# Kernel optimization log

Measured on AMD Instinct MI355X. Metric: run time of the kernel, lower is better.

## Reference

```python
import jax, jax.numpy as jnp
import numpy as np

B, N, D = 8, 4096, 256   # batch, nodes, input = hidden = output dim
TD, GD, L = 64, 73, 2    # topo_dim, gdv_dim, num_passes
NEG = -1e9               # fp32 mask value from get_mask_value


def setup_inputs() -> dict:
    key = jax.random.key(0)
    ks = jax.random.split(key, 24)
    s = 0.05
    nrm = lambda k, shp: jax.random.normal(k, shp, jnp.float32) * s
    d = {}
    d['x'] = jax.random.normal(ks[0], (B, N, D), jnp.float32)
    d['adj'] = jax.random.randint(ks[1], (D, D), 0, 2, jnp.int32)
    d['gdv'] = jax.random.uniform(ks[2], (D, GD), dtype=jnp.float32)
    d['W_in'] = nrm(ks[3], (D, D));   d['b_in'] = nrm(ks[4], (D,))
    d['W_out'] = nrm(ks[5], (D, D)); d['b_out'] = nrm(ks[6], (D,))
    d['g1_W'] = nrm(ks[7], (GD, TD));  d['g1_b'] = nrm(ks[8], (TD,))
    d['g2_W'] = nrm(ks[9], (TD, TD));  d['g2_b'] = nrm(ks[10], (TD,))
    d['gres_W'] = nrm(ks[11], (GD, TD)); d['gres_b'] = nrm(ks[12], (TD,))
    d['ln_g'] = jnp.ones((D,), jnp.float32); d['ln_b'] = jnp.zeros((D,), jnp.float32)
    d['Wf'] = nrm(ks[13], (L, D, D)); d['bf'] = nrm(ks[14], (L, D))
    d['Wt'] = nrm(ks[15], (L, TD, D)); d['bt'] = nrm(ks[16], (L, D))
    d['wa_feat'] = nrm(ks[17], (L, 2 * D)); d['ba_feat'] = nrm(ks[18], (L,))
    d['wa_topo'] = nrm(ks[19], (L, 2 * D)); d['ba_topo'] = nrm(ks[20], (L,))
    d['Wo'] = nrm(ks[21], (L, D, D)); d['bo'] = nrm(ks[22], (L, D))
    d['lng'] = jnp.ones((L, D), jnp.float32); d['lnb'] = jnp.zeros((L, D), jnp.float32)
    return d


def _ln(x, g, b, eps=1e-5):
    m = x.mean(-1, keepdims=True)
    v = ((x - m) ** 2).mean(-1, keepdims=True)
    return (x - m) * jax.lax.rsqrt(v + eps) * g + b


def reference(x, adj, gdv, W_in, b_in, W_out, b_out, g1_W, g1_b, g2_W, g2_b,
              gres_W, gres_b, ln_g, ln_b, Wf, bf, Wt, bt, wa_feat, ba_feat,
              wa_topo, ba_topo, Wo, bo, lng, lnb):
    # GDV -> topo embedding; batch-independent, so keep it [D, TD] instead of
    # the original's broadcast [B, D, TD] (same math, no duplicated compute).
    g = gdv / (gdv.sum(1, keepdims=True) + 1e-6)
    t = jax.nn.relu(g @ g1_W + g1_b) @ g2_W + g2_b + (g @ gres_W + gres_b)  # [D, TD]
    mask = adj == 0  # [D, D]
    h = x @ W_in + b_in  # [B, N, D]
    for l in range(L):
        Tp = t @ Wt[l] + bt[l]  # [D, D] topo projection (hidden_dim == D)
        # topo_attn Linear(2D,1) on cat([T_i, T_j]) == (Tp@w_i)_i + (Tp@w_j)_j + bias
        wi, wj = wa_topo[l, :D], wa_topo[l, D:]
        e_topo = jax.nn.leaky_relu((Tp @ wi)[:, None] + (Tp @ wj)[None, :] + ba_topo[l])
        beta = jax.nn.softmax(jnp.where(mask, NEG, e_topo), axis=-1)  # [D, D]
        T_out = beta @ Tp  # [D, D]
        Hp = h @ Wf[l] + bf[l]  # [B, N, D]
        # feature_attn Linear(2D,1) on cat([H_n, T_f]) decomposed the same way
        wh, wt = wa_feat[l, :D], wa_feat[l, D:]
        e_feat = jax.nn.leaky_relu((Hp @ wh)[:, :, None] + (T_out @ wt)[None, None, :] + ba_feat[l])
        alpha = jax.nn.softmax(e_feat, axis=-1)  # [B, N, D]
        h_new = jnp.einsum('bnf,fh->bnh', alpha, T_out)
        # output proj + residual (input==output -> plain add), dropout = identity (eval)
        h = _ln(h_new @ Wo[l] + bo[l] + h, lng[l], lnb[l])
    return _ln(h @ W_out + b_out, ln_g, ln_b)
```

## Files before the change

kernel.cpp:

```cpp
#include <hip/hip_runtime.h>
#include <hip/hip_bf16.h>


typedef float f32x4 __attribute__((ext_vector_type(4)));
typedef short bf16x8 __attribute__((ext_vector_type(8)));

__device__ __forceinline__ unsigned short f2bf(float f) {
  unsigned int u = __builtin_bit_cast(unsigned int, f);
  u += 0x7FFFu + ((u >> 16) & 1u);
  return (unsigned short)(u >> 16);
}
__device__ __forceinline__ float bf2f(unsigned short u) {
  return __builtin_bit_cast(float, (unsigned int)u << 16);
}
__device__ __forceinline__ float lrelu(float x) { return x > 0.f ? x : 0.01f * x; }

template <int CTRL>
__device__ __forceinline__ float dpp_ror_add(float v) {
  int s = __builtin_amdgcn_update_dpp(0, __builtin_bit_cast(int, v), CTRL, 0xf, 0xf, true);
  return v + __builtin_bit_cast(float, s);
}
__device__ __forceinline__ float sum16(float v) {
  v = dpp_ror_add<0x128>(v);
  v = dpp_ror_add<0x124>(v);
  v = dpp_ror_add<0x122>(v);
  v = dpp_ror_add<0x121>(v);
  return v;
}

__device__ __forceinline__ float block_sum(float v, float* s4, int t) {
  v = sum16(v);
  v += __shfl_xor(v, 16, 64);
  v += __shfl_xor(v, 32, 64);
  __syncthreads();
  if ((t & 63) == 0) s4[t >> 6] = v;
  __syncthreads();
  return s4[0] + s4[1] + s4[2] + s4[3];
}
__device__ __forceinline__ float block_max(float v, float* s4, int t) {
#pragma unroll
  for (int m = 1; m < 64; m <<= 1) v = fmaxf(v, __shfl_xor(v, m, 64));
  __syncthreads();
  if ((t & 63) == 0) s4[t >> 6] = v;
  __syncthreads();
  return fmaxf(fmaxf(s4[0], s4[1]), fmaxf(s4[2], s4[3]));
}

__device__ __forceinline__ int swz_off(int k, int n) {
  return ((((k >> 5) * 16 + (n >> 4)) * 4 + ((k >> 3) & 3)) * 16 + (n & 15)) * 8 + (k & 7);
}
__device__ __forceinline__ int alds_byte(int n, int m) {
  int grp = n >> 3;
  int base = (grp * 64 + m) * 16 + (n & 7) * 2;
  return base ^ ((grp & 7) << 4);
}

__global__ void ta_kernel(const float* __restrict__ gdv,
                          const float* __restrict__ g1W, const float* __restrict__ g1b,
                          const float* __restrict__ g2W, const float* __restrict__ g2b,
                          const float* __restrict__ grW, const float* __restrict__ grb,
                          const float* __restrict__ Wt, const float* __restrict__ bt,
                          const float* __restrict__ wat,
                          float* __restrict__ Tp, float* __restrict__ pb, float* __restrict__ qb) {
  int l = blockIdx.x >> 8, i = blockIdx.x & 255, t = threadIdx.x;
  __shared__ float gs[73], as_[64], ts[64], s4[4];
  float gv = (t < 73) ? gdv[i * 73 + t] : 0.f;
  float gsum = block_sum(gv, s4, t);
  if (t < 73) gs[t] = gv / (gsum + 1e-6f);
  __syncthreads();
  if (t < 64) {
    float a = g1b[t], gr = grb[t];
    for (int k = 0; k < 73; ++k) { float gk = gs[k]; a = fmaf(gk, g1W[k * 64 + t], a); gr = fmaf(gk, grW[k * 64 + t], gr); }
    as_[t] = fmaxf(a, 0.f);
    ts[t] = gr + g2b[t];
  }
  __syncthreads();
  float tv = 0.f;
  if (t < 64) {
    tv = ts[t];
    for (int k = 0; k < 64; ++k) tv = fmaf(as_[k], g2W[k * 64 + t], tv);
  }
  __syncthreads();
  if (t < 64) ts[t] = tv;
  __syncthreads();
  float tp = bt[l * 256 + t];
  for (int k = 0; k < 64; ++k) tp = fmaf(ts[k], Wt[(l * 64 + k) * 256 + t], tp);
  Tp[(l * 256 + i) * 256 + t] = tp;
  float pp = block_sum(tp * wat[l * 512 + t], s4, t);
  float qq = block_sum(tp * wat[l * 512 + 256 + t], s4, t);
  if (t == 0) { pb[l * 256 + i] = pp; qb[l * 256 + i] = qq; }
}

__global__ void tb_kernel(const int* __restrict__ adj, const float* __restrict__ Tp,
                          const float* __restrict__ pb, const float* __restrict__ qb,
                          const float* __restrict__ batopo, const float* __restrict__ Wo,
                          const float* __restrict__ wafeat, const float* __restrict__ bafeat,
                          const float* __restrict__ Wf, const float* __restrict__ bfv,
                          const float* __restrict__ Win, const float* __restrict__ Wout,
                          float* __restrict__ rp, float* __restrict__ ub, float* __restrict__ cb,
                          unsigned short* __restrict__ Uws) {
  int b = blockIdx.x, t = threadIdx.x;
  if (b >= 512) {
    int bb = b - 512;
    const float* src = (bb < 16) ? Win : Wout;
    unsigned short* dst = Uws + ((bb < 16) ? 0 : 65536);
    int r0 = (bb & 15) * 16;
    for (int kk = 0; kk < 16; ++kk) {
      int k = r0 + kk;
      dst[swz_off(k, t)] = f2bf(src[k * 256 + t]);
    }
    return;
  }
  int l = b >> 8, i = b & 255;
  __shared__ float beta[256], tout[256], s4[4];
  float e = pb[l * 256 + i] + qb[l * 256 + t] + batopo[l];
  e = lrelu(e);
  if (adj[i * 256 + t] == 0) e = -1e9f;
  float mx = block_max(e, s4, t);
  float w = __expf(e - mx);
  float Z = block_sum(w, s4, t);
  beta[t] = w / Z;
  __syncthreads();
  float acc = 0.f;
  for (int j = 0; j < 256; ++j) acc = fmaf(beta[j], Tp[(l * 256 + j) * 256 + t], acc);
  tout[t] = acc;
  __syncthreads();
  const float* WoL = Wo + l * 65536;
  float macc = 0.f;
  for (int h2 = 0; h2 < 256; ++h2) macc = fmaf(tout[h2], WoL[h2 * 256 + t], macc);
  Uws[131072 + l * 65536 + swz_off(i, t)] = f2bf(macc);
  const float* wf = wafeat + l * 512;
  float rsum = block_sum(tout[t] * wf[256 + t], s4, t);
  if (t == 0) rp[l * 256 + i] = rsum + bafeat[l];
  float usum = block_sum(Wf[(l * 256 + i) * 256 + t] * wf[t], s4, t);
  if (t == 0) ub[l * 256 + i] = usum;
  if (i == 0) {
    float csum = block_sum(bfv[l * 256 + t] * wf[t], s4, t);
    if (t == 0) cb[l] = csum;
  }
}

#define MFMA(A, B, C) __builtin_amdgcn_mfma_f32_16x16x32_bf16(A, B, C, 0, 0, 0)

__device__ __forceinline__ void kloop(const char* smc, const unsigned short* Bws,
                                      int wid, int lane, int li, int g, f32x4 acc[4][2]) {
  const bf16x8* Bw = (const bf16x8*)Bws + wid * 2 * 64 + lane;
  bf16x8 b0 = Bw[0], b1 = Bw[64];
#pragma unroll
  for (int kb = 0; kb < 8; ++kb) {
    bf16x8 nb0, nb1;
    if (kb < 7) {
      nb0 = Bw[(kb + 1) * 1024];
      nb1 = Bw[(kb + 1) * 1024 + 64];
    }
    int grp = kb * 4 + g;
    int ab = ((grp * 64 + li) * 16) ^ ((grp & 7) << 4);
    bf16x8 a0 = *(const bf16x8*)(smc + ab);
    bf16x8 a1 = *(const bf16x8*)(smc + ab + 256);
    bf16x8 a2 = *(const bf16x8*)(smc + ab + 512);
    bf16x8 a3 = *(const bf16x8*)(smc + ab + 768);
    acc[0][0] = MFMA(a0, b0, acc[0][0]);
    acc[1][0] = MFMA(a1, b0, acc[1][0]);
    acc[2][0] = MFMA(a2, b0, acc[2][0]);
    acc[3][0] = MFMA(a3, b0, acc[3][0]);
    acc[0][1] = MFMA(a0, b1, acc[0][1]);
    acc[1][1] = MFMA(a1, b1, acc[1][1]);
    acc[2][1] = MFMA(a2, b1, acc[2][1]);
    acc[3][1] = MFMA(a3, b1, acc[3][1]);
    if (kb < 7) { b0 = nb0; b1 = nb1; }
  }
}

#define S_REDUCE(UBARR, CBV)                                                   \
  {                                                                            \
    float u0_ = UBARR[ncol[0]], u1_ = UBARR[ncol[1]];                          \
    _Pragma("unroll") for (int rt = 0; rt < 4; ++rt) {                         \
      float sp[4];                                                             \
      _Pragma("unroll") for (int r = 0; r < 4; ++r)                            \
        sp[r] = h[rt][0][r] * u0_ + h[rt][1][r] * u1_;                         \
      _Pragma("unroll") for (int r = 0; r < 4; ++r) sp[r] = sum16(sp[r]);      \
      if (li == 0) {                                                           \
        _Pragma("unroll") for (int r = 0; r < 4; ++r)                          \
          red[wid][rt * 16 + g * 4 + r][0] = sp[r];                            \
      }                                                                        \
    }                                                                          \
    __syncthreads();                                                           \
    if (t < 64) {                                                              \
      float S = 0.f;                                                           \
      _Pragma("unroll") for (int w = 0; w < 8; ++w) S += red[w][t][0];         \
      row_s[t] = S + (CBV);                                                    \
    }                                                                          \
    __syncthreads();                                                           \
  }

#define LN_STATS()                                                             \
  {                                                                            \
    _Pragma("unroll") for (int rt = 0; rt < 4; ++rt) {                         \
      float sA[4], sQ[4];                                                      \
      _Pragma("unroll") for (int r = 0; r < 4; ++r) {                          \
        float a0 = h[rt][0][r], a1 = h[rt][1][r];                              \
        sA[r] = a0 + a1;                                                       \
        sQ[r] = a0 * a0 + a1 * a1;                                             \
      }                                                                        \
      _Pragma("unroll") for (int r = 0; r < 4; ++r) {                          \
        sA[r] = sum16(sA[r]); sQ[r] = sum16(sQ[r]);                            \
      }                                                                        \
      if (li == 0) {                                                           \
        _Pragma("unroll") for (int r = 0; r < 4; ++r) {                        \
          int row_ = rt * 16 + g * 4 + r;                                      \
          red[wid][row_][0] = sA[r]; red[wid][row_][1] = sQ[r];                \
        }                                                                      \
      }                                                                        \
    }                                                                          \
    __syncthreads();                                                           \
    if (t < 64) {                                                              \
      float S = 0.f, Q = 0.f;                                                  \
      _Pragma("unroll") for (int w = 0; w < 8; ++w) { S += red[w][t][0]; Q += red[w][t][1]; } \
      float mean_ = S * (1.f / 256.f);                                         \
      float var_ = Q * (1.f / 256.f) - mean_ * mean_;                          \
      mr_s[t][0] = mean_; mr_s[t][1] = rsqrtf(var_ + 1e-5f);                   \
    }                                                                          \
    __syncthreads();                                                           \
  }

__global__ void __launch_bounds__(512)
__attribute__((amdgpu_waves_per_eu(4, 4)))
fused_kernel(
    const float* __restrict__ x,
    const float* __restrict__ rp, const float* __restrict__ ub, const float* __restrict__ cbp,
    const unsigned short* __restrict__ Uws,
    const float* __restrict__ bin, const float* __restrict__ bo,
    const float* __restrict__ lng, const float* __restrict__ lnb,
    const float* __restrict__ bout, const float* __restrict__ lngf, const float* __restrict__ lnbf,
    float* __restrict__ out) {
  __shared__ unsigned short alds[18432];
  __shared__ float c_bin[256], c_bout[256], c_lngf[256], c_lnbf[256];
  __shared__ float c_ub[2][256], c_bo[2][256], c_lng[2][256], c_lnb[2][256], c_rp[2][256];
  __shared__ float red[8][64][2];
  __shared__ float row_s[64], invz_s[64];
  __shared__ float mr_s[64][2];
  __shared__ float scal_s[4];
  char* smc = (char*)alds;

  const int wg = blockIdx.x, t = threadIdx.x;
  const int wid = t >> 6, lane = t & 63, li = lane & 15, g = lane >> 4;
  const int rowbase = wg * 64;
  int ncol[2]; ncol[0] = wid * 32 + li; ncol[1] = wid * 32 + 16 + li;

  if (t < 256) {
    c_bin[t] = bin[t]; c_ub[0][t] = ub[t]; c_bo[0][t] = bo[t];
    c_lng[0][t] = lng[t]; c_lnb[0][t] = lnb[t]; c_rp[0][t] = rp[t];
  } else {
    int u = t - 256;
    c_bout[u] = bout[u]; c_lngf[u] = lngf[u]; c_lnbf[u] = lnbf[u];
    c_ub[1][u] = ub[256 + u]; c_bo[1][u] = bo[256 + u];
    c_lng[1][u] = lng[256 + u]; c_lnb[1][u] = lnb[256 + u]; c_rp[1][u] = rp[256 + u];
  }
  if (t == 0) { scal_s[2] = cbp[0]; scal_s[3] = cbp[1]; }

#pragma unroll
  for (int it = 0; it < 8; ++it) {
    int flat = it * 2048 + t * 4;
    int m = flat >> 8, col = flat & 255;
    const float4 xv = *(const float4*)(x + (rowbase + m) * 256 + col);
    ushort4 pk; pk.x = f2bf(xv.x); pk.y = f2bf(xv.y); pk.z = f2bf(xv.z); pk.w = f2bf(xv.w);
    *(ushort4*)(smc + alds_byte(col, m)) = pk;
  }
  __syncthreads();
  if (wid < 2) {
    float m2 = fmaxf(fmaxf(c_rp[wid][lane], c_rp[wid][lane + 64]),
                     fmaxf(c_rp[wid][lane + 128], c_rp[wid][lane + 192]));
#pragma unroll
    for (int mm = 1; mm < 64; mm <<= 1) m2 = fmaxf(m2, __shfl_xor(m2, mm, 64));
    if (lane == 0) scal_s[wid] = m2;
  }

  float h[4][2][4];

  {
    f32x4 acc[4][2];
#pragma unroll
    for (int a = 0; a < 4; ++a)
#pragma unroll
      for (int c = 0; c < 2; ++c) { f32x4 z = {0.f, 0.f, 0.f, 0.f}; acc[a][c] = z; }
    kloop(smc, Uws, wid, lane, li, g, acc);
#pragma unroll
    for (int rt = 0; rt < 4; ++rt)
#pragma unroll
      for (int ct = 0; ct < 2; ++ct)
#pragma unroll
        for (int r = 0; r < 4; ++r) h[rt][ct][r] = acc[rt][ct][r] + c_bin[ncol[ct]];
    S_REDUCE(c_ub[0], scal_s[2]);
  }

#pragma unroll 1
  for (int l = 0; l < 2; ++l) {
    {
      int row = t & 63;
      float sm = row_s[row];
      float mx = lrelu(sm + scal_s[l]);
      float z = 0.f;
#pragma unroll
      for (int it = 0; it < 4; ++it) {
        int grp = it * 8 + wid;
        float w0 = __expf(lrelu(sm + c_rp[l][grp * 8 + 0]) - mx);
        float w1 = __expf(lrelu(sm + c_rp[l][grp * 8 + 1]) - mx);
        float w2 = __expf(lrelu(sm + c_rp[l][grp * 8 + 2]) - mx);
        float w3 = __expf(lrelu(sm + c_rp[l][grp * 8 + 3]) - mx);
        float w4 = __expf(lrelu(sm + c_rp[l][grp * 8 + 4]) - mx);
        float w5 = __expf(lrelu(sm + c_rp[l][grp * 8 + 5]) - mx);
        float w6 = __expf(lrelu(sm + c_rp[l][grp * 8 + 6]) - mx);
        float w7 = __expf(lrelu(sm + c_rp[l][grp * 8 + 7]) - mx);
        unsigned short u0 = f2bf(w0), u1 = f2bf(w1), u2 = f2bf(w2), u3 = f2bf(w3);
        unsigned short u4 = f2bf(w4), u5 = f2bf(w5), u6 = f2bf(w6), u7 = f2bf(w7);
        z += bf2f(u0) + bf2f(u1) + bf2f(u2) + bf2f(u3) +
             bf2f(u4) + bf2f(u5) + bf2f(u6) + bf2f(u7);
        uint4 pk;
        pk.x = (unsigned int)u0 | ((unsigned int)u1 << 16);
        pk.y = (unsigned int)u2 | ((unsigned int)u3 << 16);
        pk.z = (unsigned int)u4 | ((unsigned int)u5 << 16);
        pk.w = (unsigned int)u6 | ((unsigned int)u7 << 16);
        int byte = ((grp * 64 + row) * 16) ^ ((grp & 7) << 4);
        *(uint4*)(smc + byte) = pk;
      }
      red[wid][row][0] = z;
    }
    __syncthreads();
    if (t < 64) {
      float Z = 0.f;
#pragma unroll
      for (int w = 0; w < 8; ++w) Z += red[w][t][0];
      invz_s[t] = 1.f / Z;
    }
    __syncthreads();

    f32x4 acc[4][2];
#pragma unroll
    for (int a = 0; a < 4; ++a)
#pragma unroll
      for (int c = 0; c < 2; ++c) { f32x4 z = {0.f, 0.f, 0.f, 0.f}; acc[a][c] = z; }
    kloop(smc, Uws + 131072 + l * 65536, wid, lane, li, g, acc);

#pragma unroll
    for (int rt = 0; rt < 4; ++rt)
#pragma unroll
      for (int r = 0; r < 4; ++r) {
        int row = rt * 16 + g * 4 + r;
        float iz = invz_s[row];
#pragma unroll
        for (int ct = 0; ct < 2; ++ct)
          h[rt][ct][r] = fmaf(acc[rt][ct][r], iz, c_bo[l][ncol[ct]] + h[rt][ct][r]);
      }
    LN_STATS();
#pragma unroll
    for (int rt = 0; rt < 4; ++rt)
#pragma unroll
      for (int r = 0; r < 4; ++r) {
        int row = rt * 16 + g * 4 + r;
        float mean = mr_s[row][0], rstd = mr_s[row][1];
#pragma unroll
        for (int ct = 0; ct < 2; ++ct)
          h[rt][ct][r] = (h[rt][ct][r] - mean) * rstd * c_lng[l][ncol[ct]] + c_lnb[l][ncol[ct]];
      }
    if (l == 0) S_REDUCE(c_ub[1], scal_s[3]);
  }

#pragma unroll
  for (int rt = 0; rt < 4; ++rt)
#pragma unroll
    for (int ct = 0; ct < 2; ++ct)
#pragma unroll
      for (int r = 0; r < 4; ++r) {
        int row = rt * 16 + g * 4 + r;
        *(unsigned short*)(smc + alds_byte(ncol[ct], row)) = f2bf(h[rt][ct][r]);
      }
  __syncthreads();
  {
    f32x4 acc[4][2];
#pragma unroll
    for (int a = 0; a < 4; ++a)
#pragma unroll
      for (int c = 0; c < 2; ++c) { f32x4 z = {0.f, 0.f, 0.f, 0.f}; acc[a][c] = z; }
    kloop(smc, Uws + 65536, wid, lane, li, g, acc);
#pragma unroll
    for (int rt = 0; rt < 4; ++rt)
#pragma unroll
      for (int ct = 0; ct < 2; ++ct)
#pragma unroll
        for (int r = 0; r < 4; ++r) h[rt][ct][r] = acc[rt][ct][r] + c_bout[ncol[ct]];
    LN_STATS();
#pragma unroll
    for (int rt = 0; rt < 4; ++rt)
#pragma unroll
      for (int r = 0; r < 4; ++r) {
        int row = rt * 16 + g * 4 + r;
        float mean = mr_s[row][0], rstd = mr_s[row][1];
#pragma unroll
        for (int ct = 0; ct < 2; ++ct)
          out[(rowbase + row) * 256 + ncol[ct]] =
              (h[rt][ct][r] - mean) * rstd * c_lngf[ncol[ct]] + c_lnbf[ncol[ct]];
      }
  }
}

extern "C" void kernel_launch(void* const* d_in, const int* in_sizes, int n_in,
                              void* d_out, int out_size, void* d_ws, size_t ws_size,
                              hipStream_t stream) {
  const float* x    = (const float*)d_in[0];
  const int*   adj  = (const int*)d_in[1];
  const float* gdv  = (const float*)d_in[2];
  const float* Win  = (const float*)d_in[3];
  const float* bin  = (const float*)d_in[4];
  const float* Wout = (const float*)d_in[5];
  const float* bout = (const float*)d_in[6];
  const float* g1W  = (const float*)d_in[7];
  const float* g1b  = (const float*)d_in[8];
  const float* g2W  = (const float*)d_in[9];
  const float* g2b  = (const float*)d_in[10];
  const float* grW  = (const float*)d_in[11];
  const float* grb  = (const float*)d_in[12];
  const float* lngf = (const float*)d_in[13];
  const float* lnbf = (const float*)d_in[14];
  const float* Wf   = (const float*)d_in[15];
  const float* bfv  = (const float*)d_in[16];
  const float* Wt   = (const float*)d_in[17];
  const float* bt   = (const float*)d_in[18];
  const float* waf  = (const float*)d_in[19];
  const float* baf  = (const float*)d_in[20];
  const float* wat  = (const float*)d_in[21];
  const float* bat  = (const float*)d_in[22];
  const float* Wo   = (const float*)d_in[23];
  const float* bo   = (const float*)d_in[24];
  const float* lng  = (const float*)d_in[25];
  const float* lnb  = (const float*)d_in[26];
  float* out = (float*)d_out;

  float* W = (float*)d_ws;
  float* Tp = W;
  float* pb = W + 131072;
  float* qb = W + 131584;
  float* rp = W + 132096;
  float* ub = W + 132608;
  float* cb = W + 133120;
  unsigned short* Uws = (unsigned short*)(W + 133184);

  ta_kernel<<<512, 256, 0, stream>>>(gdv, g1W, g1b, g2W, g2b, grW, grb, Wt, bt, wat, Tp, pb, qb);
  tb_kernel<<<544, 256, 0, stream>>>(adj, Tp, pb, qb, bat, Wo, waf, baf, Wf, bfv, Win, Wout, rp, ub, cb, Uws);
  fused_kernel<<<512, 512, 0, stream>>>(x, rp, ub, cb, Uws, bin, bo, lng, lnb, bout, lngf, lnbf, out);
}
```

Before: 71.29 us.

## Halve fused kernel row tile to 32 rows and double grid size

Shrinks the per-workgroup row tile of the fused kernel from 64 to 32 rows, doubling the grid to 1024 workgroups. It resizes LDS buffers, accumulators, reduction arrays and the softmax weight-building pass to match, and drops the fixed waves-per-EU attribute. The aim is more workgroups across CUs and lower register and LDS pressure per block, at the cost of loading each B weight fragment from global memory twice as often per row of output.

New measurement: 75.45 us. 5.8% more time.

```diff
diff --git a/kernel.cpp b/kernel.cpp
--- a/kernel.cpp
+++ b/kernel.cpp
@@ -51,7 +51,7 @@
 }
 __device__ __forceinline__ int alds_byte(int n, int m) {
   int grp = n >> 3;
-  int base = (grp * 64 + m) * 16 + (n & 7) * 2;
+  int base = (grp * 32 + m) * 16 + (n & 7) * 2;
   return base ^ ((grp & 7) << 4);
 }
 
@@ -143,7 +143,7 @@
 #define MFMA(A, B, C) __builtin_amdgcn_mfma_f32_16x16x32_bf16(A, B, C, 0, 0, 0)
 
 __device__ __forceinline__ void kloop(const char* smc, const unsigned short* Bws,
-                                      int wid, int lane, int li, int g, f32x4 acc[4][2]) {
+                                      int wid, int lane, int li, int g, f32x4 acc[2][2]) {
   const bf16x8* Bw = (const bf16x8*)Bws + wid * 2 * 64 + lane;
   bf16x8 b0 = Bw[0], b1 = Bw[64];
 #pragma unroll
@@ -154,19 +154,13 @@
       nb1 = Bw[(kb + 1) * 1024 + 64];
     }
     int grp = kb * 4 + g;
-    int ab = ((grp * 64 + li) * 16) ^ ((grp & 7) << 4);
+    int ab = ((grp * 32 + li) * 16) ^ ((grp & 7) << 4);
     bf16x8 a0 = *(const bf16x8*)(smc + ab);
     bf16x8 a1 = *(const bf16x8*)(smc + ab + 256);
-    bf16x8 a2 = *(const bf16x8*)(smc + ab + 512);
-    bf16x8 a3 = *(const bf16x8*)(smc + ab + 768);
     acc[0][0] = MFMA(a0, b0, acc[0][0]);
     acc[1][0] = MFMA(a1, b0, acc[1][0]);
-    acc[2][0] = MFMA(a2, b0, acc[2][0]);
-    acc[3][0] = MFMA(a3, b0, acc[3][0]);
     acc[0][1] = MFMA(a0, b1, acc[0][1]);
     acc[1][1] = MFMA(a1, b1, acc[1][1]);
-    acc[2][1] = MFMA(a2, b1, acc[2][1]);
-    acc[3][1] = MFMA(a3, b1, acc[3][1]);
     if (kb < 7) { b0 = nb0; b1 = nb1; }
   }
 }
@@ -174,20 +168,20 @@
 #define S_REDUCE(UBARR, CBV)                                                   \
   {                                                                            \
     float u0_ = UBARR[ncol[0]], u1_ = UBARR[ncol[1]];                          \
-    _Pragma("unroll") for (int rt = 0; rt < 4; ++rt) {                         \
+    _Pragma("unroll") for (int rt = 0; rt < 2; ++rt) {                         \
       float sp[4];                                                             \
       _Pragma("unroll") for (int r = 0; r < 4; ++r)                            \
         sp[r] = h[rt][0][r] * u0_ + h[rt][1][r] * u1_;                         \
       _Pragma("unroll") for (int r = 0; r < 4; ++r) sp[r] = sum16(sp[r]);      \
       if (li == 0) {                                                           \
         _Pragma("unroll") for (int r = 0; r < 4; ++r)                          \
-          red[wid][rt * 16 + g * 4 + r][0] = sp[r];                            \
+          red[wid][rt * 16 + g * 4 + r] = sp[r];                               \
       }                                                                        \
     }                                                                          \
     __syncthreads();                                                           \
-    if (t < 64) {                                                              \
+    if (t < 32) {                                                              \
       float S = 0.f;                                                           \
-      _Pragma("unroll") for (int w = 0; w < 8; ++w) S += red[w][t][0];         \
+      _Pragma("unroll") for (int w = 0; w < 8; ++w) S += red[w][t];            \
       row_s[t] = S + (CBV);                                                    \
     }                                                                          \
     __syncthreads();                                                           \
@@ -195,7 +189,7 @@
 
 #define LN_STATS()                                                             \
   {                                                                            \
-    _Pragma("unroll") for (int rt = 0; rt < 4; ++rt) {                         \
+    _Pragma("unroll") for (int rt = 0; rt < 2; ++rt) {                         \
       float sA[4], sQ[4];                                                      \
       _Pragma("unroll") for (int r = 0; r < 4; ++r) {                          \
         float a0 = h[rt][0][r], a1 = h[rt][1][r];                              \
@@ -208,14 +202,14 @@
       if (li == 0) {                                                           \
         _Pragma("unroll") for (int r = 0; r < 4; ++r) {                        \
           int row_ = rt * 16 + g * 4 + r;                                      \
-          red[wid][row_][0] = sA[r]; red[wid][row_][1] = sQ[r];                \
+          red[wid][row_] = sA[r]; red[8 + wid][row_] = sQ[r];                  \
         }                                                                      \
       }                                                                        \
     }                                                                          \
     __syncthreads();                                                           \
-    if (t < 64) {                                                              \
+    if (t < 32) {                                                              \
       float S = 0.f, Q = 0.f;                                                  \
-      _Pragma("unroll") for (int w = 0; w < 8; ++w) { S += red[w][t][0]; Q += red[w][t][1]; } \
+      _Pragma("unroll") for (int w = 0; w < 8; ++w) { S += red[w][t]; Q += red[8 + w][t]; } \
       float mean_ = S * (1.f / 256.f);                                         \
       float var_ = Q * (1.f / 256.f) - mean_ * mean_;                          \
       mr_s[t][0] = mean_; mr_s[t][1] = rsqrtf(var_ + 1e-5f);                   \
@@ -223,9 +217,7 @@
     __syncthreads();                                                           \
   }
 
-__global__ void __launch_bounds__(512)
-__attribute__((amdgpu_waves_per_eu(4, 4)))
-fused_kernel(
+__global__ __launch_bounds__(512) void fused_kernel(
     const float* __restrict__ x,
     const float* __restrict__ rp, const float* __restrict__ ub, const float* __restrict__ cbp,
     const unsigned short* __restrict__ Uws,
@@ -233,18 +225,18 @@
     const float* __restrict__ lng, const float* __restrict__ lnb,
     const float* __restrict__ bout, const float* __restrict__ lngf, const float* __restrict__ lnbf,
     float* __restrict__ out) {
-  __shared__ unsigned short alds[18432];
+  __shared__ unsigned short alds[8192];
   __shared__ float c_bin[256], c_bout[256], c_lngf[256], c_lnbf[256];
   __shared__ float c_ub[2][256], c_bo[2][256], c_lng[2][256], c_lnb[2][256], c_rp[2][256];
-  __shared__ float red[8][64][2];
-  __shared__ float row_s[64], invz_s[64];
-  __shared__ float mr_s[64][2];
+  __shared__ float red[16][32];
+  __shared__ float row_s[32], invz_s[32];
+  __shared__ float mr_s[32][2];
   __shared__ float scal_s[4];
   char* smc = (char*)alds;
 
   const int wg = blockIdx.x, t = threadIdx.x;
   const int wid = t >> 6, lane = t & 63, li = lane & 15, g = lane >> 4;
-  const int rowbase = wg * 64;
+  const int rowbase = wg * 32;
   int ncol[2]; ncol[0] = wid * 32 + li; ncol[1] = wid * 32 + 16 + li;
 
   if (t < 256) {
@@ -259,7 +251,7 @@
   if (t == 0) { scal_s[2] = cbp[0]; scal_s[3] = cbp[1]; }
 
 #pragma unroll
-  for (int it = 0; it < 8; ++it) {
+  for (int it = 0; it < 4; ++it) {
     int flat = it * 2048 + t * 4;
     int m = flat >> 8, col = flat & 255;
     const float4 xv = *(const float4*)(x + (rowbase + m) * 256 + col);
@@ -275,17 +267,17 @@
     if (lane == 0) scal_s[wid] = m2;
   }
 
-  float h[4][2][4];
+  float h[2][2][4];
 
   {
-    f32x4 acc[4][2];
-#pragma unroll
-    for (int a = 0; a < 4; ++a)
+    f32x4 acc[2][2];
+#pragma unroll
+    for (int a = 0; a < 2; ++a)
 #pragma unroll
       for (int c = 0; c < 2; ++c) { f32x4 z = {0.f, 0.f, 0.f, 0.f}; acc[a][c] = z; }
     kloop(smc, Uws, wid, lane, li, g, acc);
 #pragma unroll
-    for (int rt = 0; rt < 4; ++rt)
+    for (int rt = 0; rt < 2; ++rt)
 #pragma unroll
       for (int ct = 0; ct < 2; ++ct)
 #pragma unroll
@@ -296,13 +288,13 @@
 #pragma unroll 1
   for (int l = 0; l < 2; ++l) {
     {
-      int row = t & 63;
+      int row = t & 31, p = t >> 5;
       float sm = row_s[row];
       float mx = lrelu(sm + scal_s[l]);
       float z = 0.f;
 #pragma unroll
-      for (int it = 0; it < 4; ++it) {
-        int grp = it * 8 + wid;
+      for (int j = 0; j < 2; ++j) {
+        int grp = p * 2 + j;
         float w0 = __expf(lrelu(sm + c_rp[l][grp * 8 + 0]) - mx);
         float w1 = __expf(lrelu(sm + c_rp[l][grp * 8 + 1]) - mx);
         float w2 = __expf(lrelu(sm + c_rp[l][grp * 8 + 2]) - mx);
@@ -320,29 +312,29 @@
         pk.y = (unsigned int)u2 | ((unsigned int)u3 << 16);
         pk.z = (unsigned int)u4 | ((unsigned int)u5 << 16);
         pk.w = (unsigned int)u6 | ((unsigned int)u7 << 16);
-        int byte = ((grp * 64 + row) * 16) ^ ((grp & 7) << 4);
+        int byte = ((grp * 32 + row) * 16) ^ ((grp & 7) << 4);
         *(uint4*)(smc + byte) = pk;
       }
-      red[wid][row][0] = z;
+      red[p][row] = z;
     }
     __syncthreads();
-    if (t < 64) {
+    if (t < 32) {
       float Z = 0.f;
 #pragma unroll
-      for (int w = 0; w < 8; ++w) Z += red[w][t][0];
+      for (int p = 0; p < 16; ++p) Z += red[p][t];
       invz_s[t] = 1.f / Z;
     }
     __syncthreads();
 
-    f32x4 acc[4][2];
-#pragma unroll
-    for (int a = 0; a < 4; ++a)
+    f32x4 acc[2][2];
+#pragma unroll
+    for (int a = 0; a < 2; ++a)
 #pragma unroll
       for (int c = 0; c < 2; ++c) { f32x4 z = {0.f, 0.f, 0.f, 0.f}; acc[a][c] = z; }
     kloop(smc, Uws + 131072 + l * 65536, wid, lane, li, g, acc);
 
 #pragma unroll
-    for (int rt = 0; rt < 4; ++rt)
+    for (int rt = 0; rt < 2; ++rt)
 #pragma unroll
       for (int r = 0; r < 4; ++r) {
         int row = rt * 16 + g * 4 + r;
@@ -353,7 +345,7 @@
       }
     LN_STATS();
 #pragma unroll
-    for (int rt = 0; rt < 4; ++rt)
+    for (int rt = 0; rt < 2; ++rt)
 #pragma unroll
       for (int r = 0; r < 4; ++r) {
         int row = rt * 16 + g * 4 + r;
@@ -366,7 +358,7 @@
   }
 
 #pragma unroll
-  for (int rt = 0; rt < 4; ++rt)
+  for (int rt = 0; rt < 2; ++rt)
 #pragma unroll
     for (int ct = 0; ct < 2; ++ct)
 #pragma unroll
@@ -376,21 +368,21 @@
       }
   __syncthreads();
   {
-    f32x4 acc[4][2];
-#pragma unroll
-    for (int a = 0; a < 4; ++a)
+    f32x4 acc[2][2];
+#pragma unroll
+    for (int a = 0; a < 2; ++a)
 #pragma unroll
       for (int c = 0; c < 2; ++c) { f32x4 z = {0.f, 0.f, 0.f, 0.f}; acc[a][c] = z; }
     kloop(smc, Uws + 65536, wid, lane, li, g, acc);
 #pragma unroll
-    for (int rt = 0; rt < 4; ++rt)
+    for (int rt = 0; rt < 2; ++rt)
 #pragma unroll
       for (int ct = 0; ct < 2; ++ct)
 #pragma unroll
         for (int r = 0; r < 4; ++r) h[rt][ct][r] = acc[rt][ct][r] + c_bout[ncol[ct]];
     LN_STATS();
 #pragma unroll
-    for (int rt = 0; rt < 4; ++rt)
+    for (int rt = 0; rt < 2; ++rt)
 #pragma unroll
       for (int r = 0; r < 4; ++r) {
         int row = rt * 16 + g * 4 + r;
@@ -446,5 +438,5 @@
 
   ta_kernel<<<512, 256, 0, stream>>>(gdv, g1W, g1b, g2W, g2b, grW, grb, Wt, bt, wat, Tp, pb, qb);
   tb_kernel<<<544, 256, 0, stream>>>(adj, Tp, pb, qb, bat, Wo, waf, baf, Wf, bfv, Win, Wout, rp, ub, cb, Uws);
-  fused_kernel<<<512, 512, 0, stream>>>(x, rp, ub, cb, Uws, bin, bo, lng, lnb, bout, lngf, lnbf, out);
-}
+  fused_kernel<<<1024, 512, 0, stream>>>(x, rp, ub, cb, Uws, bin, bo, lng, lnb, bout, lngf, lnbf, out);
+}
```
